# Performance work log

Hardware: AMD Instinct MI355X
Metric: run time of the kernel (lower is better)

Reference implementation:

```python
import jax, jax.numpy as jnp
import numpy as np

B, S, H = 32, 1024, 512
NEG = -1e10

def setup_inputs() -> dict:
    key = jax.random.key(0)
    k1, k2, k3, k4, k5, k6 = jax.random.split(key, 6)
    return {
        "hidden": jax.random.normal(k1, (B, H), jnp.float32),
        "encoder_outputs": jax.random.normal(k2, (B, S, 2 * H), jnp.float32),
        "mask": jax.random.randint(k3, (B, S), 0, 2, jnp.int32),
        "W_attn": jax.random.normal(k4, (3 * H, H), jnp.float32) * (1.0 / np.sqrt(3 * H)),
        "b_attn": jax.random.normal(k5, (H,), jnp.float32) * 0.01,
        "W_v": jax.random.normal(k6, (H,), jnp.float32) * (1.0 / np.sqrt(H)),
    }

def reference(hidden, encoder_outputs, mask, W_attn, b_attn, W_v):
    # Split the concat-matmul: cat([h, enc]) @ W_attn == h @ W_h + enc @ W_e
    W_h, W_e = W_attn[:H], W_attn[H:]            # [H,H], [2H,H]
    proj_h = hidden @ W_h                        # [B, H]
    proj_e = jnp.einsum('bse,eh->bsh', encoder_outputs, W_e)  # [B, S, H]
    energy = jnp.tanh(proj_h[:, None, :] + proj_e + b_attn)   # [B, S, H]
    scores = jnp.einsum('bsh,h->bs', energy, W_v)             # [B, S]
    scores = jnp.where(mask == 0, NEG, scores)
    attn_w = jax.nn.softmax(scores, axis=1)                   # [B, S]
    context = jnp.einsum('bs,bse->be', attn_w, encoder_outputs)  # [B, 2H]
    return context, attn_w
```

## Files before the change

kernel.cpp:

```cpp
#include <hip/hip_runtime.h>
#include <hip/hip_bf16.h>
#include <math.h>

#define NB 32
#define NS 1024
#define NH 512
#define NE 1024
#define NEGV -1e10f

typedef _Float16 f16x8 __attribute__((ext_vector_type(8)));
typedef _Float16 f16x4 __attribute__((ext_vector_type(4)));
typedef float f32x4 __attribute__((ext_vector_type(4)));

__device__ __forceinline__ float fast_tanh(float x) {
  float t = __expf(2.f * x);
  return (t - 1.f) * __builtin_amdgcn_rcpf(t + 1.f);
}

__global__ __launch_bounds__(256) void proj_h_kernel(
    const float* __restrict__ hidden, const float* __restrict__ W_attn,
    const float* __restrict__ b_attn, float* __restrict__ c) {
  int b = blockIdx.x >> 1;
  int h = ((blockIdx.x & 1) << 8) + threadIdx.x;
  __shared__ float hid[NH];
  for (int e = threadIdx.x; e < NH; e += 256) hid[e] = hidden[b * NH + e];
  __syncthreads();
  float acc = b_attn[h];
#pragma unroll 8
  for (int e = 0; e < NH; ++e) acc = fmaf(hid[e], W_attn[(size_t)e * NH + h], acc);
  c[b * NH + h] = acc;
}

__global__ __launch_bounds__(256) void prep_We_kernel(
    const float* __restrict__ W_attn, _Float16* __restrict__ WeT) {
  int k = blockIdx.x;
  const float* src = W_attn + (size_t)(NH + k) * NH;
#pragma unroll
  for (int j = 0; j < 2; ++j) {
    int col = threadIdx.x + (j << 8);
    WeT[(size_t)col * NE + k] = (_Float16)src[col];
  }
}

__global__ __launch_bounds__(512, 4) void score_kernel(
    const float* __restrict__ enc, const _Float16* __restrict__ WeT,
    const float* __restrict__ c, const float* __restrict__ Wv,
    float* __restrict__ scores) {
  __shared__ float Asm[2][64 * 32];
  __shared__ _Float16 Bsm[2][512 * 32];
  const int tid = threadIdx.x;
  const int lane = tid & 63;
  const int wid = tid >> 6;
  const int r15 = lane & 15;
  const int mt = blockIdx.x;
  const int b = mt >> 4;
  const int s0 = (mt & 15) << 6;
  const char* Abase = (const char*)(enc + ((size_t)b * NS + s0) * NE);
  const char* Wbase = (const char*)WeT;

  f32x4 acc[4][4];
#pragma unroll
  for (int i = 0; i < 4; ++i)
#pragma unroll
    for (int j = 0; j < 4; ++j) acc[i][j] = (f32x4)0.f;

#define STAGE(KT, BUF)                                                           \
  {                                                                              \
    {                                                                            \
      int d = tid << 4;                                                          \
      int row = d >> 7;                                                          \
      int sb = (d & 127) ^ ((row & 7) << 4);                                     \
      __builtin_amdgcn_global_load_lds(                                          \
          (const __attribute__((address_space(1))) uint32_t*)(Abase + (size_t)row * 4096 + ((KT) << 7) + sb), \
          (__attribute__((address_space(3))) uint32_t*)((char*)Asm[BUF] + (wid << 10)), \
          16, 0, 0);                                                             \
    }                                                                            \
    _Pragma("unroll") for (int i = 0; i < 4; ++i) {                              \
      int d = (i << 13) + (tid << 4);                                            \
      int col = d >> 6;                                                          \
      int sb = (d & 63) ^ (((col >> 1) & 3) << 4);                               \
      __builtin_amdgcn_global_load_lds(                                          \
          (const __attribute__((address_space(1))) uint32_t*)(Wbase + (size_t)col * 2048 + ((KT) << 6) + sb), \
          (__attribute__((address_space(3))) uint32_t*)((char*)Bsm[BUF] + (i << 13) + (wid << 10)), \
          16, 0, 0);                                                             \
    }                                                                            \
  }

#define COMPUTE(CUR)                                                             \
  {                                                                              \
    f16x8 af[4], bf[4];                                                          \
    _Pragma("unroll") for (int mi = 0; mi < 4; ++mi) {                           \
      int row = (mi << 4) + r15;                                                 \
      int off1 = (row << 7) + ((lane >> 4) << 5);                                \
      int x = (row & 7) << 4;                                                    \
      f32x4 u = *(const f32x4*)((const char*)Asm[CUR] + (off1 ^ x));             \
      f32x4 v = *(const f32x4*)((const char*)Asm[CUR] + ((off1 + 16) ^ x));      \
      f16x8 h;                                                                   \
      h[0] = (_Float16)u[0]; h[1] = (_Float16)u[1];                              \
      h[2] = (_Float16)u[2]; h[3] = (_Float16)u[3];                              \
      h[4] = (_Float16)v[0]; h[5] = (_Float16)v[1];                              \
      h[6] = (_Float16)v[2]; h[7] = (_Float16)v[3];                              \
      af[mi] = h;                                                                \
    }                                                                            \
    _Pragma("unroll") for (int nj = 0; nj < 4; ++nj) {                           \
      int col = (wid << 6) + (nj << 4) + r15;                                    \
      int off = (col << 6) + ((lane >> 4) << 4);                                 \
      off ^= ((col >> 1) & 3) << 4;                                              \
      bf[nj] = *(const f16x8*)((const char*)Bsm[CUR] + off);                     \
    }                                                                            \
    _Pragma("unroll") for (int mi = 0; mi < 4; ++mi)                             \
      _Pragma("unroll") for (int nj = 0; nj < 4; ++nj)                           \
        acc[mi][nj] = __builtin_amdgcn_mfma_f32_16x16x32_f16(af[mi], bf[nj],     \
                                                             acc[mi][nj], 0, 0, 0); \
  }

  STAGE(0, 0);
  __syncthreads();
  for (int kt = 0; kt < 32; ++kt) {
    const int cur = kt & 1, nxt = cur ^ 1;
    if (kt < 31) STAGE(kt + 1, nxt);
    COMPUTE(cur);
    __syncthreads();
  }
#undef STAGE
#undef COMPUTE

  float sr[4][4];
#pragma unroll
  for (int i = 0; i < 4; ++i)
#pragma unroll
    for (int r = 0; r < 4; ++r) sr[i][r] = 0.f;
#pragma unroll
  for (int nj = 0; nj < 4; ++nj) {
    int hcol = (wid << 6) + (nj << 4) + r15;
    float wvj = Wv[hcol];
    float cvj = c[b * NH + hcol];
#pragma unroll
    for (int mi = 0; mi < 4; ++mi)
#pragma unroll
      for (int r = 0; r < 4; ++r)
        sr[mi][r] += wvj * fast_tanh(acc[mi][nj][r] + cvj);
  }
#pragma unroll
  for (int off = 1; off < 16; off <<= 1)
#pragma unroll
    for (int mi = 0; mi < 4; ++mi)
#pragma unroll
      for (int r = 0; r < 4; ++r) sr[mi][r] += __shfl_xor(sr[mi][r], off, 64);
  float* red = (float*)Asm;
  if (r15 == 0) {
#pragma unroll
    for (int mi = 0; mi < 4; ++mi)
#pragma unroll
      for (int r = 0; r < 4; ++r)
        red[(wid << 6) + (mi << 4) + ((lane >> 4) << 2) + r] = sr[mi][r];
  }
  __syncthreads();
  if (tid < 64) {
    float s = 0.f;
#pragma unroll
    for (int w = 0; w < 8; ++w) s += red[(w << 6) + tid];
    scores[b * NS + s0 + tid] = s;
  }
}

__global__ __launch_bounds__(256) void softmax_kernel(
    const float* __restrict__ scores, const int* __restrict__ mask,
    float* __restrict__ attn) {
  int b = blockIdx.x, tid = threadIdx.x;
  __shared__ float red[8];
  float v[4];
  float mx = -INFINITY;
#pragma unroll
  for (int j = 0; j < 4; ++j) {
    int s = tid + (j << 8);
    float x = scores[b * NS + s];
    v[j] = (mask[b * NS + s] == 0) ? NEGV : x;
    mx = fmaxf(mx, v[j]);
  }
#pragma unroll
  for (int off = 32; off >= 1; off >>= 1) mx = fmaxf(mx, __shfl_xor(mx, off, 64));
  if ((tid & 63) == 0) red[tid >> 6] = mx;
  __syncthreads();
  mx = fmaxf(fmaxf(red[0], red[1]), fmaxf(red[2], red[3]));
  float sum = 0.f;
#pragma unroll
  for (int j = 0; j < 4; ++j) {
    v[j] = __expf(v[j] - mx);
    sum += v[j];
  }
#pragma unroll
  for (int off = 32; off >= 1; off >>= 1) sum += __shfl_xor(sum, off, 64);
  __syncthreads();
  if ((tid & 63) == 0) red[4 + (tid >> 6)] = sum;
  __syncthreads();
  float inv = 1.f / (red[4] + red[5] + red[6] + red[7]);
#pragma unroll
  for (int j = 0; j < 4; ++j) attn[b * NS + tid + (j << 8)] = v[j] * inv;
}

__global__ __launch_bounds__(256) void ctx_partial_kernel(
    const float* __restrict__ enc, const float* __restrict__ attn,
    float* __restrict__ partial) {
  int ch = blockIdx.x;
  int b = blockIdx.y;
  int tid = threadIdx.x;
  __shared__ float w[64];
  if (tid < 64) w[tid] = attn[b * NS + (ch << 6) + tid];
  __syncthreads();
  const float* encb = enc + ((size_t)b * NS + (ch << 6)) * NE;
  float4 acc = make_float4(0.f, 0.f, 0.f, 0.f);
  int e = tid << 2;
  for (int s = 0; s < 64; ++s) {
    float4 x = *(const float4*)(encb + (size_t)s * NE + e);
    float ws_ = w[s];
    acc.x = fmaf(ws_, x.x, acc.x);
    acc.y = fmaf(ws_, x.y, acc.y);
    acc.z = fmaf(ws_, x.z, acc.z);
    acc.w = fmaf(ws_, x.w, acc.w);
  }
  *(float4*)(partial + ((size_t)(b * 16 + ch)) * NE + e) = acc;
}

__global__ __launch_bounds__(256) void ctx_reduce_kernel(
    const float* __restrict__ partial, float* __restrict__ ctx) {
  int b = blockIdx.x;
  int e = threadIdx.x << 2;
  float4 acc = make_float4(0.f, 0.f, 0.f, 0.f);
  for (int ch = 0; ch < 16; ++ch) {
    float4 x = *(const float4*)(partial + ((size_t)(b * 16 + ch)) * NE + e);
    acc.x += x.x;
    acc.y += x.y;
    acc.z += x.z;
    acc.w += x.w;
  }
  *(float4*)(ctx + (size_t)b * NE + e) = acc;
}

extern "C" void kernel_launch(void* const* d_in, const int* in_sizes, int n_in,
                              void* d_out, int out_size, void* d_ws, size_t ws_size,
                              hipStream_t stream) {
  const float* hidden = (const float*)d_in[0];
  const float* enc = (const float*)d_in[1];
  const int* mask = (const int*)d_in[2];
  const float* W_attn = (const float*)d_in[3];
  const float* b_attn = (const float*)d_in[4];
  const float* W_v = (const float*)d_in[5];

  float* ctx = (float*)d_out;
  float* attn = ctx + NB * NS;

  char* ws = (char*)d_ws;
  float* c = (float*)ws;
  float* scores = (float*)(ws + 65536);
  float* partial = (float*)(ws + 65536 + 131072);
  _Float16* WeT = (_Float16*)(ws + 65536 + 131072 + 2097152);

  proj_h_kernel<<<64, 256, 0, stream>>>(hidden, W_attn, b_attn, c);
  prep_We_kernel<<<NE, 256, 0, stream>>>(W_attn, WeT);
  score_kernel<<<512, 512, 0, stream>>>(enc, WeT, c, W_v, scores);
  softmax_kernel<<<NB, 256, 0, stream>>>(scores, mask, attn);
  ctx_partial_kernel<<<dim3(16, NB), 256, 0, stream>>>(enc, attn, partial);
  ctx_reduce_kernel<<<NB, 256, 0, stream>>>(partial, ctx);
}
```

Measured before the change: 115.8 us.

## Split score GEMM across two H-halves with partial-score buffers reduced in softmax

The score kernel now runs 1024 blocks of 256 threads, each covering half of the H columns, instead of 512 blocks of 512 threads. Each wave writes its own partial row-score vector to a workspace, and the softmax kernel sums the 8 partials, which removes the in-block LDS reduction. Block IDs are remapped so neighbouring blocks use different batch and sequence tiles. The aim is more blocks and smaller LDS per block for better occupancy, at the cost of each encoder tile being loaded and converted twice and more global traffic for partial scores.

After: 135.6 us. 1.17x slower.

```diff
diff --git a/kernel.cpp b/kernel.cpp
--- a/kernel.cpp
+++ b/kernel.cpp
@@ -42,21 +42,23 @@
   }
 }
 
-__global__ __launch_bounds__(512, 4) void score_kernel(
+__global__ __launch_bounds__(256, 3) void score_kernel(
     const float* __restrict__ enc, const _Float16* __restrict__ WeT,
     const float* __restrict__ c, const float* __restrict__ Wv,
-    float* __restrict__ scores) {
+    float* __restrict__ spart) {
   __shared__ float Asm[2][64 * 32];
-  __shared__ _Float16 Bsm[2][512 * 32];
+  __shared__ _Float16 Bsm[2][256 * 32];
   const int tid = threadIdx.x;
   const int lane = tid & 63;
-  const int wid = tid >> 6;
+  const int wc = tid >> 6;
   const int r15 = lane & 15;
-  const int mt = blockIdx.x;
-  const int b = mt >> 4;
-  const int s0 = (mt & 15) << 6;
+  const int id = blockIdx.x;
+  const int lb = ((id & 7) << 6) + (id >> 3);
+  const int b = lb >> 4;
+  const int s0 = (lb & 15) << 6;
+  const int nc = blockIdx.y;
   const char* Abase = (const char*)(enc + ((size_t)b * NS + s0) * NE);
-  const char* Wbase = (const char*)WeT;
+  const char* Wbase = (const char*)(WeT + ((size_t)(nc << 8)) * NE);
 
   f32x4 acc[4][4];
 #pragma unroll
@@ -66,22 +68,22 @@
 
 #define STAGE(KT, BUF)                                                           \
   {                                                                              \
-    {                                                                            \
-      int d = tid << 4;                                                          \
+    _Pragma("unroll") for (int p = 0; p < 2; ++p) {                              \
+      int d = (p << 12) + (tid << 4);                                            \
       int row = d >> 7;                                                          \
       int sb = (d & 127) ^ ((row & 7) << 4);                                     \
       __builtin_amdgcn_global_load_lds(                                          \
           (const __attribute__((address_space(1))) uint32_t*)(Abase + (size_t)row * 4096 + ((KT) << 7) + sb), \
-          (__attribute__((address_space(3))) uint32_t*)((char*)Asm[BUF] + (wid << 10)), \
+          (__attribute__((address_space(3))) uint32_t*)((char*)Asm[BUF] + (p << 12) + (wc << 10)), \
           16, 0, 0);                                                             \
     }                                                                            \
-    _Pragma("unroll") for (int i = 0; i < 4; ++i) {                              \
-      int d = (i << 13) + (tid << 4);                                            \
+    _Pragma("unroll") for (int p = 0; p < 4; ++p) {                              \
+      int d = (p << 12) + (tid << 4);                                            \
       int col = d >> 6;                                                          \
       int sb = (d & 63) ^ (((col >> 1) & 3) << 4);                               \
       __builtin_amdgcn_global_load_lds(                                          \
           (const __attribute__((address_space(1))) uint32_t*)(Wbase + (size_t)col * 2048 + ((KT) << 6) + sb), \
-          (__attribute__((address_space(3))) uint32_t*)((char*)Bsm[BUF] + (i << 13) + (wid << 10)), \
+          (__attribute__((address_space(3))) uint32_t*)((char*)Bsm[BUF] + (p << 12) + (wc << 10)), \
           16, 0, 0);                                                             \
     }                                                                            \
   }
@@ -103,7 +105,7 @@
       af[mi] = h;                                                                \
     }                                                                            \
     _Pragma("unroll") for (int nj = 0; nj < 4; ++nj) {                           \
-      int col = (wid << 6) + (nj << 4) + r15;                                    \
+      int col = (wc << 6) + (nj << 4) + r15;                                     \
       int off = (col << 6) + ((lane >> 4) << 4);                                 \
       off ^= ((col >> 1) & 3) << 4;                                              \
       bf[nj] = *(const f16x8*)((const char*)Bsm[CUR] + off);                     \
@@ -132,7 +134,7 @@
     for (int r = 0; r < 4; ++r) sr[i][r] = 0.f;
 #pragma unroll
   for (int nj = 0; nj < 4; ++nj) {
-    int hcol = (wid << 6) + (nj << 4) + r15;
+    int hcol = (nc << 8) + (wc << 6) + (nj << 4) + r15;
     float wvj = Wv[hcol];
     float cvj = c[b * NH + hcol];
 #pragma unroll
@@ -147,25 +149,18 @@
     for (int mi = 0; mi < 4; ++mi)
 #pragma unroll
       for (int r = 0; r < 4; ++r) sr[mi][r] += __shfl_xor(sr[mi][r], off, 64);
-  float* red = (float*)Asm;
   if (r15 == 0) {
+    float* dst = spart + (size_t)((nc << 2) + wc) * NB * NS + b * NS + s0;
 #pragma unroll
     for (int mi = 0; mi < 4; ++mi)
 #pragma unroll
       for (int r = 0; r < 4; ++r)
-        red[(wid << 6) + (mi << 4) + ((lane >> 4) << 2) + r] = sr[mi][r];
-  }
-  __syncthreads();
-  if (tid < 64) {
-    float s = 0.f;
-#pragma unroll
-    for (int w = 0; w < 8; ++w) s += red[(w << 6) + tid];
-    scores[b * NS + s0 + tid] = s;
+        dst[(mi << 4) + ((lane >> 4) << 2) + r] = sr[mi][r];
   }
 }
 
 __global__ __launch_bounds__(256) void softmax_kernel(
-    const float* __restrict__ scores, const int* __restrict__ mask,
+    const float* __restrict__ spart, const int* __restrict__ mask,
     float* __restrict__ attn) {
   int b = blockIdx.x, tid = threadIdx.x;
   __shared__ float red[8];
@@ -174,7 +169,9 @@
 #pragma unroll
   for (int j = 0; j < 4; ++j) {
     int s = tid + (j << 8);
-    float x = scores[b * NS + s];
+    float x = 0.f;
+#pragma unroll
+    for (int p = 0; p < 8; ++p) x += spart[(size_t)p * NB * NS + b * NS + s];
     v[j] = (mask[b * NS + s] == 0) ? NEGV : x;
     mx = fmaxf(mx, v[j]);
   }
@@ -252,14 +249,14 @@
 
   char* ws = (char*)d_ws;
   float* c = (float*)ws;
-  float* scores = (float*)(ws + 65536);
-  float* partial = (float*)(ws + 65536 + 131072);
-  _Float16* WeT = (_Float16*)(ws + 65536 + 131072 + 2097152);
+  float* spart = (float*)(ws + 65536);
+  float* partial = (float*)(ws + 65536 + 1048576);
+  _Float16* WeT = (_Float16*)(ws + 65536 + 1048576 + 2097152);
 
   proj_h_kernel<<<64, 256, 0, stream>>>(hidden, W_attn, b_attn, c);
   prep_We_kernel<<<NE, 256, 0, stream>>>(W_attn, WeT);
-  score_kernel<<<512, 512, 0, stream>>>(enc, WeT, c, W_v, scores);
-  softmax_kernel<<<NB, 256, 0, stream>>>(scores, mask, attn);
+  score_kernel<<<dim3(512, 2), 256, 0, stream>>>(enc, WeT, c, W_v, spart);
+  softmax_kernel<<<NB, 256, 0, stream>>>(spart, mask, attn);
   ctx_partial_kernel<<<dim3(16, NB), 256, 0, stream>>>(enc, attn, partial);
   ctx_reduce_kernel<<<NB, 256, 0, stream>>>(partial, ctx);
 }
```
